# Performance work log

Hardware: AMD Instinct MI355X
Metric: run time of the kernel (lower is better)

The kernel has to match this reference:

```python
import jax, jax.numpy as jnp
import numpy as np

EPS = 1e-5


def setup_inputs() -> dict:
    key = jax.random.key(0)
    ks = jax.random.split(key, 8)
    B, C, D, H, O, E = 256, 64, 256, 4096, 256, 4
    x = jax.random.normal(ks[0], (B, C, D), dtype=jnp.float32)
    mask_ids = jax.random.randint(ks[1], (B, C), 0, 16)
    projection_idx = jax.random.randint(ks[2], (C,), 0, E)
    W1 = jax.random.normal(ks[3], (E, D, H), dtype=jnp.float32) * 0.02
    b1 = jnp.zeros((E, H), dtype=jnp.float32)
    gamma = jnp.ones((E, H), dtype=jnp.float32)
    beta = jnp.zeros((E, H), dtype=jnp.float32)
    W2 = jax.random.normal(ks[4], (E, H, O), dtype=jnp.float32) * 0.02
    b2 = jnp.zeros((E, O), dtype=jnp.float32)
    return {"x": x, "mask_ids": mask_ids, "projection_idx": projection_idx,
            "W1": W1, "b1": b1, "gamma": gamma, "beta": beta, "W2": W2, "b2": b2}


def reference(x, mask_ids, projection_idx, W1, b1, gamma, beta, W2, b2):
    # x: [B, C, D]; projection_idx: [C] routes each channel to one of E experts.
    # Disjoint masks => the original zeros + masked '+=' is a partition-assign.
    B, C, D = x.shape
    E, _, H = W1.shape
    # Per-channel expert params (gather once, shared over batch).
    h = jnp.einsum('bcd,cdh->bch', x, W1[projection_idx]) + b1[projection_idx]
    # BatchNorm1d in training mode: batch stats over the tokens of each expert
    # (the original flattens the selected [B, |mask|] tokens for BN).
    seg = jnp.broadcast_to(projection_idx[None, :], (B, C)).reshape(-1)  # [B*C]
    hf = h.reshape(B * C, H)
    cnt = jax.ops.segment_sum(jnp.ones((B * C,), h.dtype), seg, num_segments=E)
    cnt = jnp.maximum(cnt, 1.0)
    s1 = jax.ops.segment_sum(hf, seg, num_segments=E)            # [E, H]
    s2 = jax.ops.segment_sum(hf * hf, seg, num_segments=E)       # [E, H]
    mean = s1 / cnt[:, None]
    var = s2 / cnt[:, None] - mean * mean                        # biased var (train-mode BN)
    inv = jax.lax.rsqrt(var + EPS)
    hn = (h - mean[projection_idx]) * (inv[projection_idx] * gamma[projection_idx]) + beta[projection_idx]
    a = jax.nn.relu(hn)
    out = jnp.einsum('bch,cho->bco', a, W2[projection_idx]) + b2[projection_idx]
    return out, mask_ids
```

## Files before the change

kernel.cpp:

```cpp
#include <hip/hip_runtime.h>

typedef unsigned short u16;
typedef unsigned int   u32;
typedef __attribute__((ext_vector_type(8))) short s16x8;
typedef __attribute__((ext_vector_type(4))) float f32x4;
typedef __attribute__((ext_vector_type(4))) u32   u32x4;

#define DEV static __device__ __forceinline__

static constexpr int B_ = 256, C_ = 64, D_ = 256, H_ = 4096, O_ = 256, E_ = 4;

DEV u16 f2bf(float f) {
  u32 u = __builtin_bit_cast(u32, f);
  u += 0x7fffu + ((u >> 16) & 1u);
  return (u16)(u >> 16);
}
DEV float bf2f(u16 u) { return __builtin_bit_cast(float, (u32)u << 16); }

DEV void async16(const u16* g, u16* l) {
  __builtin_amdgcn_global_load_lds(
      (const __attribute__((address_space(1))) void*)g,
      (__attribute__((address_space(3))) void*)l, 16, 0, 0);
}

DEV int xcd_swz(int bid, int nwg) { return (bid & 7) * (nwg >> 3) + (bid >> 3); }

__global__ void k_cvt(const float* __restrict__ src, u16* __restrict__ dst) {
  const int i = blockIdx.x * blockDim.x + threadIdx.x;
  const f32x4 a = ((const f32x4*)src)[2 * i];
  const f32x4 b = ((const f32x4*)src)[2 * i + 1];
  u32x4 o;
  o[0] = (u32)f2bf(a[0]) | ((u32)f2bf(a[1]) << 16);
  o[1] = (u32)f2bf(a[2]) | ((u32)f2bf(a[3]) << 16);
  o[2] = (u32)f2bf(b[0]) | ((u32)f2bf(b[1]) << 16);
  o[3] = (u32)f2bf(b[2]) | ((u32)f2bf(b[3]) << 16);
  ((u32x4*)dst)[i] = o;
}

__global__ void k_transpose(const float* __restrict__ src, u16* __restrict__ dst,
                            const int R, const int Cc) {
  __shared__ float tile[64][65];
  const int nct = Cc >> 6, nrt = R >> 6;
  int bx = blockIdx.x;
  const int ct = bx % nct; bx /= nct;
  const int rt = bx % nrt; const int e = bx / nrt;
  const float* s = src + (size_t)e * R * Cc;
  u16* d = dst + (size_t)e * R * Cc;
  const int tx = threadIdx.x & 63, ty = threadIdx.x >> 6;
  #pragma unroll
  for (int i = 0; i < 64; i += 4)
    tile[i + ty][tx] = s[(size_t)(rt * 64 + i + ty) * Cc + ct * 64 + tx];
  __syncthreads();
  #pragma unroll
  for (int i = 0; i < 64; i += 4) {
    const int cc = i + ty;
    d[(size_t)(ct * 64 + cc) * R + rt * 64 + tx] = f2bf(tile[tx][cc]);
  }
}

__global__ void k_sortc(const int* __restrict__ proj, int* __restrict__ perm) {
  const int c = threadIdx.x;
  const int e = proj[c];
  int rank = 0;
  for (int c2 = 0; c2 < C_; ++c2) {
    const int e2 = proj[c2];
    rank += (e2 < e) || (e2 == e && c2 < c);
  }
  perm[rank] = c;
}

__global__ __launch_bounds__(256, 2)
void k_gemm1(const u16* __restrict__ A, const u16* __restrict__ Bw,
             const int* __restrict__ proj, const int* __restrict__ perm,
             const float* __restrict__ bias,
             u16* __restrict__ outH, float* __restrict__ s1g, float* __restrict__ s2g) {
  constexpr int BM = 128, BN = 128, BK = 64, KT = D_ / BK;
  constexpr int SA = BM * BK / 8, SB = BN * BK / 8;
  constexpr int BUF = (SA + SB) * 8;
  __shared__ __align__(16) u16 lds[2 * BUF];
  const int tid = threadIdx.x, l = tid & 63, w = tid >> 6, wm = w >> 1, wn = w & 1;

  int bid = xcd_swz(blockIdx.x, gridDim.x);
  constexpr int NT = H_ / BN, BT = B_ / BM;
  const int nt = bid % NT; bid /= NT;
  const int bt = bid % BT; const int ci = bid / BT;
  const int c = perm[ci];
  const int e = proj[c];

  const size_t rsA = (size_t)C_ * D_;
  const u16* Ab = A + (size_t)c * D_ + (size_t)bt * BM * rsA;
  const u16* Bb = Bw + ((size_t)e * H_ + (size_t)nt * BN) * D_;

  f32x4 acc[4][4] = {};

  auto stage = [&](int kt) {
    const int k0 = kt * BK;
    u16* dst = lds + (kt & 1) * BUF;
    #pragma unroll
    for (int i = 0; i < SA / 256; ++i) {
      const int s = i * 256 + tid, row = s >> 3, j = (s & 7) ^ (row & 7);
      async16(Ab + (size_t)row * rsA + k0 + j * 8, dst + s * 8);
    }
    #pragma unroll
    for (int i = 0; i < SB / 256; ++i) {
      const int s = i * 256 + tid, col = s >> 3, j = (s & 7) ^ (col & 7);
      async16(Bb + (size_t)col * D_ + k0 + j * 8, dst + SA * 8 + s * 8);
    }
  };

  stage(0);
  asm volatile("s_waitcnt vmcnt(0)" ::: "memory");
  __builtin_amdgcn_s_barrier();

  #pragma unroll
  for (int kt = 0; kt < KT; ++kt) {
    if (kt + 1 < KT) stage(kt + 1);
    const u16* bufA = lds + (kt & 1) * BUF;
    const u16* bufB = bufA + SA * 8;
    s16x8 av[2][4], bv[2][4];
    #pragma unroll
    for (int kk = 0; kk < 2; ++kk) {
      #pragma unroll
      for (int m = 0; m < 4; ++m) {
        const int r = wm * 64 + m * 16 + (l & 15), p = (kk * 4 + (l >> 4)) ^ (r & 7);
        av[kk][m] = *(const s16x8*)(bufA + (r * 8 + p) * 8);
      }
      #pragma unroll
      for (int n = 0; n < 4; ++n) {
        const int cc = wn * 64 + n * 16 + (l & 15), p = (kk * 4 + (l >> 4)) ^ (cc & 7);
        bv[kk][n] = *(const s16x8*)(bufB + (cc * 8 + p) * 8);
      }
    }
    #pragma unroll
    for (int kk = 0; kk < 2; ++kk)
      #pragma unroll
      for (int m = 0; m < 4; ++m)
        #pragma unroll
        for (int n = 0; n < 4; ++n)
          acc[m][n] = __builtin_amdgcn_mfma_f32_16x16x32_bf16(av[kk][m], bv[kk][n], acc[m][n], 0, 0, 0);
    asm volatile("s_waitcnt vmcnt(0) lgkmcnt(0)" ::: "memory");
    __builtin_amdgcn_s_barrier();
  }

  u16* ldsOut = lds;
  #pragma unroll
  for (int n = 0; n < 4; ++n) {
    const int colL = wn * 64 + n * 16 + (l & 15);
    const int colg = nt * BN + colL;
    const float bval = bias[e * H_ + colg];
    float p1 = 0.f, p2 = 0.f;
    #pragma unroll
    for (int m = 0; m < 4; ++m) {
      const int rbase = wm * 64 + m * 16 + (l >> 4) * 4;
      #pragma unroll
      for (int i = 0; i < 4; ++i) {
        const float v = acc[m][n][i] + bval;
        p1 += v; p2 += v * v;
        const int row = rbase + i;
        const int phys = (colL >> 3) ^ (row & 15);
        ldsOut[row * 128 + phys * 8 + (colL & 7)] = f2bf(v);
      }
    }
    p1 += __shfl_xor(p1, 16); p1 += __shfl_xor(p1, 32);
    p2 += __shfl_xor(p2, 16); p2 += __shfl_xor(p2, 32);
    if (l < 16) {
      atomicAdd(&s1g[e * H_ + colg], p1);
      atomicAdd(&s2g[e * H_ + colg], p2);
    }
  }
  __syncthreads();
  u16* outB = outH + ((size_t)(bt * BM) * C_ + c) * H_ + nt * BN;
  #pragma unroll
  for (int pass = 0; pass < 8; ++pass) {
    const int row = pass * 16 + (tid >> 4), sl = tid & 15;
    const u32x4 v = *(const u32x4*)(ldsOut + row * 128 + ((sl ^ (row & 15)) * 8));
    *(u32x4*)(outB + (size_t)row * C_ * H_ + sl * 8) = v;
  }
}

__global__ void k_finalize(const float* __restrict__ s1, const float* __restrict__ s2,
                           const int* __restrict__ proj, const float* __restrict__ gamma,
                           const float* __restrict__ beta,
                           u16* __restrict__ sclB, u16* __restrict__ shfB) {
  const int i = blockIdx.x * 256 + threadIdx.x;
  const int e = i >> 12;
  int cn = 0;
  #pragma unroll
  for (int c = 0; c < C_; ++c) cn += (proj[c] == e) ? 1 : 0;
  const float cnt = fmaxf((float)cn * (float)B_, 1.f);
  const float mean = s1[i] / cnt;
  const float var = s2[i] / cnt - mean * mean;
  const float sc = rsqrtf(var + 1e-5f) * gamma[i];
  sclB[i] = f2bf(sc);
  shfB[i] = f2bf(beta[i] - mean * sc);
}

__global__ __launch_bounds__(256, 1)
void k_gemm2(const u16* __restrict__ A, const u16* __restrict__ Bw,
             const int* __restrict__ proj, const int* __restrict__ perm,
             const float* __restrict__ b2,
             const u16* __restrict__ scB, const u16* __restrict__ shB,
             float* __restrict__ outF) {
  constexpr int BM = 64, BN = 256, BK = 64, KT = H_ / BK;
  constexpr int SA = BM * BK / 8, SB = BN * BK / 8;
  constexpr int BUF = (SA + SB) * 8;
  __shared__ __align__(16) u16 lds[2 * BUF];
  const int tid = threadIdx.x, l = tid & 63, w = tid >> 6;

  int bid = xcd_swz(blockIdx.x, gridDim.x);
  const int bt = bid % (B_ / BM); const int ci = bid / (B_ / BM);
  const int c = perm[ci];
  const int e = proj[c];

  const size_t rsA = (size_t)C_ * H_;
  const u16* Ab = A + (size_t)c * H_ + (size_t)bt * BM * rsA;
  const u16* Bb = Bw + (size_t)e * O_ * H_;
  const u16* scE = scB + e * H_;
  const u16* shE = shB + e * H_;

  f32x4 acc[4][4] = {};
  s16x8 hA[2], sA[2], tA[2];

  auto Aissue = [&](int kt) {
    const int k0 = kt * BK;
    #pragma unroll
    for (int i = 0; i < 2; ++i) {
      const int s = i * 256 + tid, row = s >> 3, j = (s & 7) ^ (row & 7), k = k0 + j * 8;
      hA[i] = *(const s16x8*)(Ab + (size_t)row * rsA + k);
      sA[i] = *(const s16x8*)(scE + k);
      tA[i] = *(const s16x8*)(shE + k);
    }
  };
  auto Bissue = [&](int kt) {
    const int k0 = kt * BK;
    u16* dst = lds + (kt & 1) * BUF + SA * 8;
    #pragma unroll
    for (int i = 0; i < 8; ++i) {
      const int s = i * 256 + tid, col = s >> 3, j = (s & 7) ^ (col & 7);
      async16(Bb + (size_t)col * H_ + k0 + j * 8, dst + s * 8);
    }
  };
  auto Awrite = [&](int kt) {
    u16* dst = lds + (kt & 1) * BUF;
    #pragma unroll
    for (int i = 0; i < 2; ++i) {
      const int s = i * 256 + tid;
      u32x4 o;
      #pragma unroll
      for (int jj = 0; jj < 4; ++jj) {
        const float v0 = fmaxf(bf2f((u16)hA[i][2 * jj]) * bf2f((u16)sA[i][2 * jj]) + bf2f((u16)tA[i][2 * jj]), 0.f);
        const float v1 = fmaxf(bf2f((u16)hA[i][2 * jj + 1]) * bf2f((u16)sA[i][2 * jj + 1]) + bf2f((u16)tA[i][2 * jj + 1]), 0.f);
        o[jj] = (u32)f2bf(v0) | ((u32)f2bf(v1) << 16);
      }
      *(u32x4*)(dst + s * 8) = o;
    }
  };

  Aissue(0); Bissue(0); Awrite(0);
  asm volatile("s_waitcnt vmcnt(0) lgkmcnt(0)" ::: "memory");
  __builtin_amdgcn_s_barrier();

  #pragma unroll 2
  for (int kt = 0; kt < KT; ++kt) {
    if (kt + 1 < KT) { Aissue(kt + 1); Bissue(kt + 1); }
    const u16* bufA = lds + (kt & 1) * BUF;
    const u16* bufB = bufA + SA * 8;
    s16x8 av[2][4], bv[2][4];
    #pragma unroll
    for (int kk = 0; kk < 2; ++kk) {
      #pragma unroll
      for (int m = 0; m < 4; ++m) {
        const int r = m * 16 + (l & 15), p = (kk * 4 + (l >> 4)) ^ (r & 7);
        av[kk][m] = *(const s16x8*)(bufA + (r * 8 + p) * 8);
      }
      #pragma unroll
      for (int n = 0; n < 4; ++n) {
        const int cc = w * 64 + n * 16 + (l & 15), p = (kk * 4 + (l >> 4)) ^ (cc & 7);
        bv[kk][n] = *(const s16x8*)(bufB + (cc * 8 + p) * 8);
      }
    }
    #pragma unroll
    for (int kk = 0; kk < 2; ++kk)
      #pragma unroll
      for (int m = 0; m < 4; ++m)
        #pragma unroll
        for (int n = 0; n < 4; ++n)
          acc[m][n] = __builtin_amdgcn_mfma_f32_16x16x32_bf16(av[kk][m], bv[kk][n], acc[m][n], 0, 0, 0);
    if (kt + 1 < KT) Awrite(kt + 1);
    asm volatile("s_waitcnt vmcnt(0) lgkmcnt(0)" ::: "memory");
    __builtin_amdgcn_s_barrier();
  }

  #pragma unroll
  for (int n = 0; n < 4; ++n) {
    const int colg = w * 64 + n * 16 + (l & 15);
    const float bval = b2[e * O_ + colg];
    #pragma unroll
    for (int m = 0; m < 4; ++m) {
      #pragma unroll
      for (int i = 0; i < 4; ++i) {
        const int rg = bt * BM + m * 16 + (l >> 4) * 4 + i;
        outF[((size_t)rg * C_ + c) * O_ + colg] = acc[m][n][i] + bval;
      }
    }
  }
}

__global__ void k_mask(const int* __restrict__ m, float* __restrict__ o) {
  const int i = blockIdx.x * 256 + threadIdx.x;
  o[i] = (float)m[i];
}

extern "C" void kernel_launch(void* const* d_in, const int* in_sizes, int n_in,
                              void* d_out, int out_size, void* d_ws, size_t ws_size,
                              hipStream_t stream) {
  const float* x     = (const float*)d_in[0];
  const int*   mask  = (const int*)d_in[1];
  const int*   proj  = (const int*)d_in[2];
  const float* W1    = (const float*)d_in[3];
  const float* b1    = (const float*)d_in[4];
  const float* gamma = (const float*)d_in[5];
  const float* beta  = (const float*)d_in[6];
  const float* W2    = (const float*)d_in[7];
  const float* b2    = (const float*)d_in[8];
  float* out = (float*)d_out;

  char* ws = (char*)d_ws;
  size_t off = 0;
  u16* hbuf = (u16*)(ws + off); off += (size_t)B_ * C_ * H_ * 2;
  u16* xb   = (u16*)(ws + off); off += (size_t)B_ * C_ * D_ * 2;
  u16* w1t  = (u16*)(ws + off); off += (size_t)E_ * D_ * H_ * 2;
  u16* w2t  = (u16*)(ws + off); off += (size_t)E_ * H_ * O_ * 2;
  float* s1 = (float*)(ws + off); off += (size_t)E_ * H_ * 4;
  float* s2 = (float*)(ws + off); off += (size_t)E_ * H_ * 4;
  u16* sclB = (u16*)(ws + off); off += (size_t)E_ * H_ * 2;
  u16* shfB = (u16*)(ws + off); off += (size_t)E_ * H_ * 2;
  int* perm = (int*)(ws + off); off += 256;

  (void)hipMemsetAsync(s1, 0, (size_t)2 * E_ * H_ * 4, stream);

  k_sortc<<<1, 64, 0, stream>>>(proj, perm);
  k_cvt<<<2048, 256, 0, stream>>>(x, xb);
  k_transpose<<<E_ * 4 * 64, 256, 0, stream>>>(W1, w1t, D_, H_);
  k_transpose<<<E_ * 64 * 4, 256, 0, stream>>>(W2, w2t, H_, O_);

  k_gemm1<<<C_ * 2 * 32, 256, 0, stream>>>(xb, w1t, proj, perm, b1, hbuf, s1, s2);

  k_finalize<<<E_ * H_ / 256, 256, 0, stream>>>(s1, s2, proj, gamma, beta, sclB, shfB);

  k_gemm2<<<C_ * 4, 256, 0, stream>>>(hbuf, w2t, proj, perm, b2, sclB, shfB, out);

  k_mask<<<B_ * C_ / 256, 256, 0, stream>>>(mask, out + (size_t)B_ * C_ * O_);
}
```

Measured before the change: 182.1 us.

## Split-K second GEMM with partial-sum combine, shrink first GEMM K-tile for occupancy

The second GEMM goes from a 256-block grid (one block per channel and batch slice) to 512 blocks. It uses 128x128 tiles and splits the H reduction in half. The second half writes to a partial buffer that reuses the dead x-bf16 workspace, and a new combine kernel adds it into the output and also converts the mask. The first GEMM halves its K-tile to 32 to cut LDS use and raises its launch-bounds occupancy target from 2 to 4. In exchange the change adds an extra fp32 read/write pass over the output, and the first GEMM runs more barriers per K.

```diff
diff --git a/kernel.cpp b/kernel.cpp
--- a/kernel.cpp
+++ b/kernel.cpp
@@ -69,12 +69,12 @@
   perm[rank] = c;
 }
 
-__global__ __launch_bounds__(256, 2)
+__global__ __launch_bounds__(256, 4)
 void k_gemm1(const u16* __restrict__ A, const u16* __restrict__ Bw,
              const int* __restrict__ proj, const int* __restrict__ perm,
              const float* __restrict__ bias,
              u16* __restrict__ outH, float* __restrict__ s1g, float* __restrict__ s2g) {
-  constexpr int BM = 128, BN = 128, BK = 64, KT = D_ / BK;
+  constexpr int BM = 128, BN = 128, BK = 32, KT = D_ / BK;
   constexpr int SA = BM * BK / 8, SB = BN * BK / 8;
   constexpr int BUF = (SA + SB) * 8;
   __shared__ __align__(16) u16 lds[2 * BUF];
@@ -98,12 +98,12 @@
     u16* dst = lds + (kt & 1) * BUF;
     #pragma unroll
     for (int i = 0; i < SA / 256; ++i) {
-      const int s = i * 256 + tid, row = s >> 3, j = (s & 7) ^ (row & 7);
+      const int s = i * 256 + tid, row = s >> 2, j = (s & 3) ^ (row & 3);
       async16(Ab + (size_t)row * rsA + k0 + j * 8, dst + s * 8);
     }
     #pragma unroll
     for (int i = 0; i < SB / 256; ++i) {
-      const int s = i * 256 + tid, col = s >> 3, j = (s & 7) ^ (col & 7);
+      const int s = i * 256 + tid, col = s >> 2, j = (s & 3) ^ (col & 3);
       async16(Bb + (size_t)col * D_ + k0 + j * 8, dst + SA * 8 + s * 8);
     }
   };
@@ -117,27 +117,22 @@
     if (kt + 1 < KT) stage(kt + 1);
     const u16* bufA = lds + (kt & 1) * BUF;
     const u16* bufB = bufA + SA * 8;
-    s16x8 av[2][4], bv[2][4];
-    #pragma unroll
-    for (int kk = 0; kk < 2; ++kk) {
-      #pragma unroll
-      for (int m = 0; m < 4; ++m) {
-        const int r = wm * 64 + m * 16 + (l & 15), p = (kk * 4 + (l >> 4)) ^ (r & 7);
-        av[kk][m] = *(const s16x8*)(bufA + (r * 8 + p) * 8);
-      }
-      #pragma unroll
-      for (int n = 0; n < 4; ++n) {
-        const int cc = wn * 64 + n * 16 + (l & 15), p = (kk * 4 + (l >> 4)) ^ (cc & 7);
-        bv[kk][n] = *(const s16x8*)(bufB + (cc * 8 + p) * 8);
-      }
-    }
-    #pragma unroll
-    for (int kk = 0; kk < 2; ++kk)
-      #pragma unroll
-      for (int m = 0; m < 4; ++m)
-        #pragma unroll
-        for (int n = 0; n < 4; ++n)
-          acc[m][n] = __builtin_amdgcn_mfma_f32_16x16x32_bf16(av[kk][m], bv[kk][n], acc[m][n], 0, 0, 0);
+    s16x8 av[4], bv[4];
+    #pragma unroll
+    for (int m = 0; m < 4; ++m) {
+      const int r = wm * 64 + m * 16 + (l & 15), p = (l >> 4) ^ (r & 3);
+      av[m] = *(const s16x8*)(bufA + (r * 4 + p) * 8);
+    }
+    #pragma unroll
+    for (int n = 0; n < 4; ++n) {
+      const int cc = wn * 64 + n * 16 + (l & 15), p = (l >> 4) ^ (cc & 3);
+      bv[n] = *(const s16x8*)(bufB + (cc * 4 + p) * 8);
+    }
+    #pragma unroll
+    for (int m = 0; m < 4; ++m)
+      #pragma unroll
+      for (int n = 0; n < 4; ++n)
+        acc[m][n] = __builtin_amdgcn_mfma_f32_16x16x32_bf16(av[m], bv[n], acc[m][n], 0, 0, 0);
     asm volatile("s_waitcnt vmcnt(0) lgkmcnt(0)" ::: "memory");
     __builtin_amdgcn_s_barrier();
   }
@@ -195,36 +190,38 @@
   shfB[i] = f2bf(beta[i] - mean * sc);
 }
 
-__global__ __launch_bounds__(256, 1)
+__global__ __launch_bounds__(256, 2)
 void k_gemm2(const u16* __restrict__ A, const u16* __restrict__ Bw,
              const int* __restrict__ proj, const int* __restrict__ perm,
              const float* __restrict__ b2,
              const u16* __restrict__ scB, const u16* __restrict__ shB,
-             float* __restrict__ outF) {
-  constexpr int BM = 64, BN = 256, BK = 64, KT = H_ / BK;
+             float* __restrict__ outF, float* __restrict__ partial) {
+  constexpr int BM = 128, BN = 128, BK = 64, KH = H_ / 2, KT = KH / BK;
   constexpr int SA = BM * BK / 8, SB = BN * BK / 8;
   constexpr int BUF = (SA + SB) * 8;
   __shared__ __align__(16) u16 lds[2 * BUF];
-  const int tid = threadIdx.x, l = tid & 63, w = tid >> 6;
+  const int tid = threadIdx.x, l = tid & 63, w = tid >> 6, wm = w >> 1, wn = w & 1;
 
   int bid = xcd_swz(blockIdx.x, gridDim.x);
-  const int bt = bid % (B_ / BM); const int ci = bid / (B_ / BM);
+  const int ks = bid & 1; bid >>= 1;
+  const int nt = bid & 1; bid >>= 1;
+  const int bt = bid & 1; const int ci = bid >> 1;
   const int c = perm[ci];
   const int e = proj[c];
 
   const size_t rsA = (size_t)C_ * H_;
-  const u16* Ab = A + (size_t)c * H_ + (size_t)bt * BM * rsA;
-  const u16* Bb = Bw + (size_t)e * O_ * H_;
-  const u16* scE = scB + e * H_;
-  const u16* shE = shB + e * H_;
+  const u16* Ab = A + (size_t)c * H_ + (size_t)bt * BM * rsA + (size_t)ks * KH;
+  const u16* Bb = Bw + ((size_t)e * O_ + (size_t)nt * BN) * H_ + (size_t)ks * KH;
+  const u16* scE = scB + e * H_ + ks * KH;
+  const u16* shE = shB + e * H_ + ks * KH;
 
   f32x4 acc[4][4] = {};
-  s16x8 hA[2], sA[2], tA[2];
+  s16x8 hA[4], sA[4], tA[4];
 
   auto Aissue = [&](int kt) {
     const int k0 = kt * BK;
     #pragma unroll
-    for (int i = 0; i < 2; ++i) {
+    for (int i = 0; i < 4; ++i) {
       const int s = i * 256 + tid, row = s >> 3, j = (s & 7) ^ (row & 7), k = k0 + j * 8;
       hA[i] = *(const s16x8*)(Ab + (size_t)row * rsA + k);
       sA[i] = *(const s16x8*)(scE + k);
@@ -235,7 +232,7 @@
     const int k0 = kt * BK;
     u16* dst = lds + (kt & 1) * BUF + SA * 8;
     #pragma unroll
-    for (int i = 0; i < 8; ++i) {
+    for (int i = 0; i < 4; ++i) {
       const int s = i * 256 + tid, col = s >> 3, j = (s & 7) ^ (col & 7);
       async16(Bb + (size_t)col * H_ + k0 + j * 8, dst + s * 8);
     }
@@ -243,7 +240,7 @@
   auto Awrite = [&](int kt) {
     u16* dst = lds + (kt & 1) * BUF;
     #pragma unroll
-    for (int i = 0; i < 2; ++i) {
+    for (int i = 0; i < 4; ++i) {
       const int s = i * 256 + tid;
       u32x4 o;
       #pragma unroll
@@ -270,12 +267,12 @@
     for (int kk = 0; kk < 2; ++kk) {
       #pragma unroll
       for (int m = 0; m < 4; ++m) {
-        const int r = m * 16 + (l & 15), p = (kk * 4 + (l >> 4)) ^ (r & 7);
+        const int r = wm * 64 + m * 16 + (l & 15), p = (kk * 4 + (l >> 4)) ^ (r & 7);
         av[kk][m] = *(const s16x8*)(bufA + (r * 8 + p) * 8);
       }
       #pragma unroll
       for (int n = 0; n < 4; ++n) {
-        const int cc = w * 64 + n * 16 + (l & 15), p = (kk * 4 + (l >> 4)) ^ (cc & 7);
+        const int cc = wn * 64 + n * 16 + (l & 15), p = (kk * 4 + (l >> 4)) ^ (cc & 7);
         bv[kk][n] = *(const s16x8*)(bufB + (cc * 8 + p) * 8);
       }
     }
@@ -291,24 +288,35 @@
     __builtin_amdgcn_s_barrier();
   }
 
+  float* dstF = ks ? partial : outF;
   #pragma unroll
   for (int n = 0; n < 4; ++n) {
-    const int colg = w * 64 + n * 16 + (l & 15);
-    const float bval = b2[e * O_ + colg];
+    const int colg = nt * BN + wn * 64 + n * 16 + (l & 15);
+    const float bval = ks ? 0.f : b2[e * O_ + colg];
     #pragma unroll
     for (int m = 0; m < 4; ++m) {
       #pragma unroll
       for (int i = 0; i < 4; ++i) {
-        const int rg = bt * BM + m * 16 + (l >> 4) * 4 + i;
-        outF[((size_t)rg * C_ + c) * O_ + colg] = acc[m][n][i] + bval;
-      }
-    }
-  }
-}
-
-__global__ void k_mask(const int* __restrict__ m, float* __restrict__ o) {
-  const int i = blockIdx.x * 256 + threadIdx.x;
-  o[i] = (float)m[i];
+        const int rg = bt * BM + wm * 64 + m * 16 + (l >> 4) * 4 + i;
+        dstF[((size_t)rg * C_ + c) * O_ + colg] = acc[m][n][i] + bval;
+      }
+    }
+  }
+}
+
+__global__ void k_combine(float* __restrict__ out, const float* __restrict__ partial,
+                          const int* __restrict__ mask, float* __restrict__ maskOut) {
+  const int gi = blockIdx.x * 256 + threadIdx.x;
+  const size_t b = (size_t)gi * 2;
+  f32x4 a0 = ((const f32x4*)out)[b],     a1 = ((const f32x4*)out)[b + 1];
+  const f32x4 p0 = ((const f32x4*)partial)[b], p1 = ((const f32x4*)partial)[b + 1];
+  #pragma unroll
+  for (int j = 0; j < 4; ++j) { a0[j] += p0[j]; a1[j] += p1[j]; }
+  ((f32x4*)out)[b] = a0; ((f32x4*)out)[b + 1] = a1;
+  if (gi < B_ * C_ / 8) {
+    #pragma unroll
+    for (int j = 0; j < 8; ++j) maskOut[gi * 8 + j] = (float)mask[gi * 8 + j];
+  }
 }
 
 extern "C" void kernel_launch(void* const* d_in, const int* in_sizes, int n_in,
@@ -330,6 +338,7 @@
   u16* hbuf = (u16*)(ws + off); off += (size_t)B_ * C_ * H_ * 2;
   u16* xb   = (u16*)(ws + off); off += (size_t)B_ * C_ * D_ * 2;
   u16* w1t  = (u16*)(ws + off); off += (size_t)E_ * D_ * H_ * 2;
+  float* partial = (float*)xb;
   u16* w2t  = (u16*)(ws + off); off += (size_t)E_ * H_ * O_ * 2;
   float* s1 = (float*)(ws + off); off += (size_t)E_ * H_ * 4;
   float* s2 = (float*)(ws + off); off += (size_t)E_ * H_ * 4;
@@ -348,7 +357,8 @@
 
   k_finalize<<<E_ * H_ / 256, 256, 0, stream>>>(s1, s2, proj, gamma, beta, sclB, shfB);
 
-  k_gemm2<<<C_ * 4, 256, 0, stream>>>(hbuf, w2t, proj, perm, b2, sclB, shfB, out);
-
-  k_mask<<<B_ * C_ / 256, 256, 0, stream>>>(mask, out + (size_t)B_ * C_ * O_);
-}
+  k_gemm2<<<512, 256, 0, stream>>>(hbuf, w2t, proj, perm, b2, sclB, shfB, out, partial);
+
+  k_combine<<<B_ * C_ * O_ / 8 / 256, 256, 0, stream>>>(out, partial, mask,
+                                                        out + (size_t)B_ * C_ * O_);
+}
```

After: 160.3 us. 1.14x faster.
